# Optimization experiments

Hardware: AMD Instinct MI355X
Metric: run time of the kernel (lower is better)

Reference implementation:

```python
import jax, jax.numpy as jnp
import numpy as np

DIM = 256
NUM_HEADS = 8
NUM_NEI = (16, 32)
G = len(NUM_NEI)          # branches
G_H = NUM_HEADS // G      # heads per branch = 4
G_DIM = DIM // G          # channels per branch = 128
HD = G_DIM // G_H         # head dim = 32
SCALE = HD ** (-0.5)
M_MSF = G                 # MSF branches
CHANNEL = DIM // M_MSF    # 128
D_MSF = CHANNEL           # r=1

gelu = lambda t: jax.nn.gelu(t, approximate=False)


def setup_inputs() -> dict:
    key = jax.random.key(0)
    ks = jax.random.split(key, 16)
    B, N = 4, 2048
    s = lambda fan: fan ** (-0.5)
    inp = {
        "x": jax.random.normal(ks[0], (B, N, DIM), jnp.float32),
        "pos": jax.random.uniform(ks[1], (B, N, 3), jnp.float32),
        # qkv linear (no bias); stored as (in, out)
        "Wqkv": jax.random.normal(ks[2], (DIM, 3 * DIM), jnp.float32) * s(DIM),
        # per-branch rel-pos MLPs: Linear(3, g_dim) + GELU
        "Wp0": jax.random.normal(ks[3], (3, G_DIM), jnp.float32) * s(3),
        "bp0": jnp.zeros((G_DIM,), jnp.float32),
        "Wp1": jax.random.normal(ks[4], (3, G_DIM), jnp.float32) * s(3),
        "bp1": jnp.zeros((G_DIM,), jnp.float32),
        # MSF params
        "W_proj": jax.random.normal(ks[5], (DIM, DIM), jnp.float32) * s(DIM),
        "b_proj": jnp.zeros((DIM,), jnp.float32),
        "W_fc1": jax.random.normal(ks[6], (DIM, D_MSF), jnp.float32) * s(DIM),
        "b_fc1": jnp.zeros((D_MSF,), jnp.float32),
        "W_fc2": jax.random.normal(ks[7], (D_MSF, M_MSF * CHANNEL), jnp.float32) * s(D_MSF),
        "b_fc2": jnp.zeros((M_MSF * CHANNEL,), jnp.float32),
        "W_head": jax.random.normal(ks[8], (DIM, DIM), jnp.float32) * s(DIM),
        "b_head": jnp.zeros((DIM,), jnp.float32),
    }
    return inp


def _branch(q, k, v, pos, knn_idx, Wp, bp):
    """One head-group: KNN gather + rel-pos MLP fused attention.
    q,k,v: [B,N,g_dim]; pos: [B,N,3]; knn_idx: [B,N,nk]."""
    B, N, g_dim = k.shape
    nk = knn_idx.shape[-1]
    gather = jax.vmap(lambda t, idx: t[idx])  # per-batch fancy gather -> [B,N,nk,D]
    knn_xyz = gather(pos, knn_idx)                       # [B,N,nk,3]
    kg = gather(k, knn_idx)                              # [B,N,nk,g_dim]
    vg = gather(v, knn_idx)
    # split heads: b n k (h d) -> b h n k d
    split = lambda t: t.reshape(B, N, nk, G_H, HD).transpose(0, 3, 1, 2, 4)
    kg, vg = split(kg), split(vg)
    rel = pos[:, :, None, :] - knn_xyz                   # [B,N,nk,3]
    vrp = split(gelu(rel @ Wp + bp))                     # [B,h,N,nk,d]
    vg = vg + vrp
    attn_rel = vrp.sum(-1)                               # [B,h,N,nk]
    qh = q.reshape(B, N, G_H, HD).transpose(0, 2, 1, 3)  # [B,h,N,d]
    logits = jnp.einsum('bhnd,bhnkd->bhnk', qh, kg) * SCALE + attn_rel
    a = jax.nn.softmax(logits, axis=-1)
    out = jnp.einsum('bhnk,bhnkd->bhnd', a, vg)          # [B,h,N,d]
    return out.transpose(0, 2, 1, 3).reshape(B, N, g_dim)


def _msf(x, W_proj, b_proj, W_fc1, b_fc1, W_fc2, b_fc2, W_head, b_head):
    bs, N, dim = x.shape
    input_groups = x.transpose(0, 2, 1).reshape(bs, M_MSF, CHANNEL, N)
    feats_proj = gelu(x @ W_proj + b_proj)               # [bs,N,dim]
    feats_S = feats_proj.mean(axis=1)                    # global avg pool over N -> [bs,dim]
    feats_Z = gelu(feats_S @ W_fc1 + b_fc1)
    av = (feats_Z @ W_fc2 + b_fc2).reshape(bs, M_MSF, CHANNEL, 1)
    av = jax.nn.softmax(av, axis=1)                      # softmax over branches
    feats_V = (input_groups * av).reshape(bs, dim, N).transpose(0, 2, 1)
    feats_V = feats_V @ W_head + b_head
    return feats_proj + feats_V


def reference(x, pos, Wqkv, Wp0, bp0, Wp1, bp1,
              W_proj, b_proj, W_fc1, b_fc1, W_fc2, b_fc2, W_head, b_head):
    B, N, C = x.shape
    # pairwise squared distances [B,N,N] (broadcast form, as in source)
    dists = jnp.sum((pos[:, :, None, :] - pos[:, None, :, :]) ** 2, axis=-1)
    order = jnp.argsort(dists, axis=-1)                  # [B,N,N]
    qkv = (x @ Wqkv).reshape(B, N, 3, C).transpose(2, 0, 1, 3)  # [3,B,N,C]
    pos_params = [(Wp0, bp0), (Wp1, bp1)]
    outs = []
    for i, nk in enumerate(NUM_NEI):
        sl = slice(i * G_DIM, (i + 1) * G_DIM)
        q, k, v = qkv[0][..., sl], qkv[1][..., sl], qkv[2][..., sl]
        knn_idx = order[:, :, :nk]
        Wp, bp = pos_params[i]
        outs.append(_branch(q, k, v, pos, knn_idx, Wp, bp))
    xcat = jnp.concatenate(outs, axis=-1)                # [B,N,C]
    return _msf(xcat, W_proj, b_proj, W_fc1, b_fc1, W_fc2, b_fc2, W_head, b_head)
```

## Files before the change

### kernel.cpp

```cpp
#include <hip/hip_runtime.h>
#include <cstdint>
#include <cstddef>

#define B_    4
#define NPT   2048
#define DIM_  256
#define QKVW  768
#define XLEN  2097152
#define QLEN  196608
#define PLEN  65536
#define TOTC  (XLEN + QLEN + 2 * PLEN)

typedef unsigned short ushort_t;
typedef unsigned long long u64;
typedef short bf16x8 __attribute__((ext_vector_type(8)));
typedef float f32x4 __attribute__((ext_vector_type(4)));

__device__ __forceinline__ float gelu_f(float x) {
  return 0.5f * x * (1.0f + erff(x * 0.70710678118654752440f));
}

__device__ __forceinline__ float gelu_fast(float x) {
  const float is2 = 0.70710678118654752440f;
  float z = x * is2;
  float az = __builtin_fabsf(z);
  float t = __builtin_amdgcn_rcpf(fmaf(0.3275911f, az, 1.0f));
  float p = fmaf(1.061405429f, t, -1.453152027f);
  p = fmaf(p, t, 1.421413741f);
  p = fmaf(p, t, -0.284496736f);
  p = fmaf(p, t, 0.254829592f);
  p = p * t;
  float e = __expf(-az * az);
  float er = fmaf(-p, e, 1.0f);
  er = __builtin_copysignf(er, x);
  return 0.5f * x * (1.0f + er);
}

__device__ __forceinline__ ushort_t f2bf(float f) {
  unsigned u = __float_as_uint(f);
  unsigned r = (u + 0x7fffu + ((u >> 16) & 1u)) >> 16;
  return (ushort_t)r;
}
__device__ __forceinline__ float bf2f(ushort_t h) {
  return __uint_as_float(((unsigned)h) << 16);
}

__device__ __forceinline__ float bfly16_sum(float x) {
  x += __int_as_float(__builtin_amdgcn_ds_swizzle(__float_as_int(x), 0x041F));
  x += __int_as_float(__builtin_amdgcn_ds_swizzle(__float_as_int(x), 0x081F));
  x += __int_as_float(__builtin_amdgcn_ds_swizzle(__float_as_int(x), 0x101F));
  x += __int_as_float(__builtin_amdgcn_ds_swizzle(__float_as_int(x), 0x201F));
  return x;
}

__device__ __forceinline__ bf16x8 scale_bf(bf16x8 v, const float* avk) {
  bf16x8 r;
#pragma unroll
  for (int e = 0; e < 8; e++) {
    float f = bf2f((ushort_t)v[e]) * avk[e];
    r[e] = (short)f2bf(f);
  }
  return r;
}

__global__ __launch_bounds__(256) void convert_kernel(
    const float* __restrict__ x, const float* __restrict__ Wqkv,
    const float* __restrict__ Wproj, const float* __restrict__ Whead,
    ushort_t* __restrict__ xbf, ushort_t* __restrict__ WqkvT,
    ushort_t* __restrict__ WprojT, ushort_t* __restrict__ WheadT,
    float* __restrict__ part) {
  int base = blockIdx.x * 256 + threadIdx.x;
  if (base < 1024) part[base] = 0.f;
  for (int i = base; i < TOTC; i += 2048 * 256) {
    if (i < XLEN) {
      xbf[i] = f2bf(x[i]);
    } else if (i < XLEN + QLEN) {
      int e = i - XLEN;
      int k = e / 768, n = e - k * 768;
      WqkvT[n * 256 + k] = f2bf(Wqkv[e]);
    } else if (i < XLEN + QLEN + PLEN) {
      int e = i - XLEN - QLEN;
      int k = e >> 8, n = e & 255;
      WprojT[n * 256 + k] = f2bf(Wproj[e]);
    } else {
      int e = i - XLEN - QLEN - PLEN;
      int k = e >> 8, n = e & 255;
      WheadT[n * 256 + k] = f2bf(Whead[e]);
    }
  }
}

__global__ __launch_bounds__(256) void knn_gemm0_kernel(
    const float* __restrict__ pos, int* __restrict__ idx_out,
    const ushort_t* __restrict__ A, const ushort_t* __restrict__ BT,
    float* __restrict__ C) {
  __shared__ u64 buf[4][128];
  int tid = threadIdx.x;
  int w = tid >> 6, lane = tid & 63;
  if (blockIdx.x >= 2048) {
    constexpr int K = 256;
    constexpr int N = 768;
    int quad = lane >> 4, r16 = lane & 15;
    int t0 = (blockIdx.x - 2048) * 4 + w;
    int m0 = (t0 / 24) * 64, n0 = (t0 % 24) * 32;
    const ushort_t* Ap = A + (size_t)(m0 + r16) * K + quad * 8;
    const ushort_t* Bp = BT + (size_t)(n0 + r16) * K + quad * 8;
    f32x4 acc[4][2] = {};
    bf16x8 af[4], bfv[2], af2[4], bf2[2];
#pragma unroll
    for (int i = 0; i < 4; i++) af[i] = *(const bf16x8*)(Ap + (size_t)i * 16 * K);
#pragma unroll
    for (int j = 0; j < 2; j++) bfv[j] = *(const bf16x8*)(Bp + (size_t)j * 16 * K);
#pragma unroll
    for (int kc = 0; kc < 8; kc++) {
      if (kc < 7) {
        int ko = (kc + 1) * 32;
#pragma unroll
        for (int i = 0; i < 4; i++)
          af2[i] = *(const bf16x8*)(Ap + (size_t)i * 16 * K + ko);
#pragma unroll
        for (int j = 0; j < 2; j++)
          bf2[j] = *(const bf16x8*)(Bp + (size_t)j * 16 * K + ko);
      }
#pragma unroll
      for (int i = 0; i < 4; i++) {
        acc[i][0] = __builtin_amdgcn_mfma_f32_16x16x32_bf16(af[i], bfv[0], acc[i][0], 0, 0, 0);
        acc[i][1] = __builtin_amdgcn_mfma_f32_16x16x32_bf16(af[i], bfv[1], acc[i][1], 0, 0, 0);
      }
#pragma unroll
      for (int i = 0; i < 4; i++) af[i] = af2[i];
      bfv[0] = bf2[0]; bfv[1] = bf2[1];
    }
#pragma unroll
    for (int i = 0; i < 4; i++) {
#pragma unroll
      for (int j = 0; j < 2; j++) {
        int col = n0 + j * 16 + r16;
#pragma unroll
        for (int r = 0; r < 4; r++) {
          int row = m0 + i * 16 + quad * 4 + r;
          C[(size_t)row * N + col] = acc[i][j][r];
        }
      }
    }
    return;
  }
  int wq = blockIdx.x * 4 + w;
  int b = wq >> 11, n = wq & (NPT - 1);
  const float* pb = pos + (size_t)b * NPT * 3;
  float qx = pb[n * 3 + 0], qy = pb[n * 3 + 1], qz = pb[n * 3 + 2];
  float dist[32];
  {
#pragma clang fp contract(off)
#pragma unroll
    for (int s = 0; s < 32; s++) {
      int j = lane + (s << 6);
      float dx = qx - pb[j * 3 + 0];
      float dy = qy - pb[j * 3 + 1];
      float dz = qz - pb[j * 3 + 2];
      float d = dx * dx;
      d = d + dy * dy;
      d = d + dz * dz;
      dist[s] = d;
    }
  }
  unsigned lo = 0x3C000000u;
  unsigned hi = 0x3E800001u;
  for (int it = 0; it < 31 && hi - lo > 1; ++it) {
    unsigned mid = (lo + hi) >> 1;
    float fm = __uint_as_float(mid);
    int c = 0;
#pragma unroll
    for (int s = 0; s < 32; s++)
      c += (int)__popcll(__ballot(dist[s] < fm));
    if (c >= 32) { hi = mid; if (c <= 64) break; }
    else lo = mid;
  }
  float fT = __uint_as_float(hi);
  buf[w][lane] = ~0ULL;
  buf[w][lane + 64] = ~0ULL;
  __builtin_amdgcn_wave_barrier();
  asm volatile("s_waitcnt lgkmcnt(0)" ::: "memory");
  unsigned base = 0;
#pragma unroll
  for (int s = 0; s < 32; s++) {
    bool m = dist[s] < fT;
    u64 bal = __ballot(m);
    unsigned pre = __builtin_amdgcn_mbcnt_hi(
        (unsigned)(bal >> 32), __builtin_amdgcn_mbcnt_lo((unsigned)bal, 0u));
    unsigned p = base + pre;
    if (m && p < 128u) {
      int j = lane + (s << 6);
      buf[w][p] = ((u64)__float_as_uint(dist[s]) << 32) | (unsigned)j;
    }
    base += (unsigned)__popcll(bal);
  }
  __builtin_amdgcn_wave_barrier();
  asm volatile("s_waitcnt lgkmcnt(0)" ::: "memory");
  unsigned total = base;
  if (total > 128u) total = 128u;
  unsigned mt = (total + 7u) & ~7u;
  u64 k0 = buf[w][lane];
  u64 k1 = buf[w][lane + 64];
  int r0 = 0, r1 = 0;
  for (unsigned i = 0; i < mt; i += 8) {
#pragma unroll
    for (int t = 0; t < 8; t++) {
      u64 ki = buf[w][i + t];
      r0 += (ki < k0) ? 1 : 0;
      r1 += (ki < k1) ? 1 : 0;
    }
  }
  if (r0 < 32) idx_out[(size_t)wq * 32 + r0] = (int)(unsigned)(k0 & 0xffffffffULL);
  if (r1 < 32) idx_out[(size_t)wq * 32 + r1] = (int)(unsigned)(k1 & 0xffffffffULL);
}

template <int MODE>
__global__ __launch_bounds__(64, 4) void gemm_rf(
    const ushort_t* __restrict__ A, const ushort_t* __restrict__ BT,
    const float* __restrict__ bias, const float* __restrict__ extra,
    float* __restrict__ C, float* __restrict__ part,
    const float* __restrict__ av, int N) {
  constexpr int K = 256;
  int lane = threadIdx.x;
  int quad = lane >> 4, r16 = lane & 15;
  int t0 = blockIdx.x;
  int m0 = (t0 >> 3) * 64, n0 = (t0 & 7) * 32;
  int batch = m0 >> 11;
  const ushort_t* Ap = A + (size_t)(m0 + r16) * K + quad * 8;
  const ushort_t* Bp = BT + (size_t)(n0 + r16) * K + quad * 8;
  f32x4 acc[4][2] = {};
  bf16x8 af[4], bf[2], af2[4], bf2[2];
#pragma unroll
  for (int i = 0; i < 4; i++) af[i] = *(const bf16x8*)(Ap + (size_t)i * 16 * K);
#pragma unroll
  for (int j = 0; j < 2; j++) bf[j] = *(const bf16x8*)(Bp + (size_t)j * 16 * K);
#pragma unroll
  for (int kc = 0; kc < 8; kc++) {
    if (kc < 7) {
      int ko = (kc + 1) * 32;
#pragma unroll
      for (int i = 0; i < 4; i++)
        af2[i] = *(const bf16x8*)(Ap + (size_t)i * 16 * K + ko);
#pragma unroll
      for (int j = 0; j < 2; j++)
        bf2[j] = *(const bf16x8*)(Bp + (size_t)j * 16 * K + ko);
    }
    bf16x8 b0 = bf[0], b1 = bf[1];
    if (MODE == 2) {
      const float* avk = av + batch * 256 + kc * 32 + quad * 8;
      b0 = scale_bf(b0, avk);
      b1 = scale_bf(b1, avk);
    }
#pragma unroll
    for (int i = 0; i < 4; i++) {
      acc[i][0] = __builtin_amdgcn_mfma_f32_16x16x32_bf16(af[i], b0, acc[i][0], 0, 0, 0);
      acc[i][1] = __builtin_amdgcn_mfma_f32_16x16x32_bf16(af[i], b1, acc[i][1], 0, 0, 0);
    }
#pragma unroll
    for (int i = 0; i < 4; i++) af[i] = af2[i];
    bf[0] = bf2[0]; bf[1] = bf2[1];
  }
  float cs[2] = {};
#pragma unroll
  for (int i = 0; i < 4; i++) {
#pragma unroll
    for (int j = 0; j < 2; j++) {
      int col = n0 + j * 16 + r16;
#pragma unroll
      for (int r = 0; r < 4; r++) {
        int row = m0 + i * 16 + quad * 4 + r;
        float v = acc[i][j][r];
        if (MODE == 1) { v = gelu_fast(v + bias[col]); cs[j] += v; }
        else if (MODE == 2) v = extra[(size_t)row * 256 + col] + v + bias[col];
        C[(size_t)row * N + col] = v;
      }
    }
  }
  if (MODE == 1) {
#pragma unroll
    for (int j = 0; j < 2; j++) {
      cs[j] += __shfl_xor(cs[j], 16, 64);
      cs[j] += __shfl_xor(cs[j], 32, 64);
    }
    if (quad == 0) {
#pragma unroll
      for (int j = 0; j < 2; j++)
        atomicAdd(&part[batch * 256 + n0 + j * 16 + r16], cs[j]);
    }
  }
}

template <int NK>
__device__ __forceinline__ void attn_core(
    const float* __restrict__ kvbase, int c2, const int* sidx,
    const float4* srel, float qSx, float qSy,
    float2 w0, float2 w1, float2 w2, float2 bb,
    float& num0, float& num1, float& den) {
#pragma unroll
  for (int j = 0; j < NK; j++) {
    int jj = __builtin_amdgcn_readfirstlane(sidx[j]);
    float4 rr = srel[j];
    const float* kb = kvbase + (size_t)jj * QKVW;
    float2 kv = *(const float2*)(kb + c2);
    float2 vv = *(const float2*)(kb + 256 + c2);
    float x0 = fmaf(rr.x, w0.x, fmaf(rr.y, w1.x, fmaf(rr.z, w2.x, bb.x)));
    float x1 = fmaf(rr.x, w0.y, fmaf(rr.y, w1.y, fmaf(rr.z, w2.y, bb.y)));
    float z0 = x0 * fmaf(0.0713548163f, x0 * x0, 1.5957691216f);
    float z1 = x1 * fmaf(0.0713548163f, x1 * x1, 1.5957691216f);
    float r0 = x0 * __builtin_amdgcn_rcpf(1.0f + __expf(-z0));
    float r1 = x1 * __builtin_amdgcn_rcpf(1.0f + __expf(-z1));
    float p = fmaf(qSx, kv.x, r0) + fmaf(qSy, kv.y, r1);
    float logit = bfly16_sum(p);
    float e = __expf(logit);
    den += e;
    num0 = fmaf(e, vv.x + r0, num0);
    num1 = fmaf(e, vv.y + r1, num1);
  }
}

__global__ __launch_bounds__(64) void attn_kernel(
    const float* __restrict__ qkv, const float* __restrict__ pos,
    const int* __restrict__ knn,
    const float* __restrict__ Wp0, const float* __restrict__ bp0,
    const float* __restrict__ Wp1, const float* __restrict__ bp1,
    ushort_t* __restrict__ xcat) {
  const float SCALE = 0.17677669529663687f;
  int u = blockIdx.x;
  int g = blockIdx.y;
  int b = u >> 11, n = u & (NPT - 1);
  int lane = threadIdx.x;
  int c2 = lane * 2;
  __shared__ int s_idx[32];
  __shared__ float4 s_rel[32];
  const float* qkvb = qkv + (size_t)b * NPT * QKVW;
  if (lane < 32) {
    int j = knn[(size_t)u * 32 + lane];
    s_idx[lane] = j;
    const float* pn = pos + ((size_t)b * NPT + n) * 3;
    const float* pj = pos + ((size_t)b * NPT + j) * 3;
    s_rel[lane] = make_float4(pn[0] - pj[0], pn[1] - pj[1],
                              pn[2] - pj[2], 0.f);
  }
  __builtin_amdgcn_wave_barrier();
  asm volatile("s_waitcnt lgkmcnt(0)" ::: "memory");
  const float* Wp = g ? Wp1 : Wp0;
  const float* bp = g ? bp1 : bp0;
  float2 w0 = *(const float2*)(Wp + c2);
  float2 w1 = *(const float2*)(Wp + 128 + c2);
  float2 w2 = *(const float2*)(Wp + 256 + c2);
  float2 bb = *(const float2*)(bp + c2);
  float2 q2 = *(const float2*)(qkvb + (size_t)n * QKVW + g * 128 + c2);
  float qSx = q2.x * SCALE, qSy = q2.y * SCALE;
  const float* kvbase = qkvb + 256 + g * 128;
  float num0 = 0.f, num1 = 0.f, den = 0.f;
  if (g == 0)
    attn_core<16>(kvbase, c2, s_idx, s_rel, qSx, qSy, w0, w1, w2, bb,
                  num0, num1, den);
  else
    attn_core<32>(kvbase, c2, s_idx, s_rel, qSx, qSy, w0, w1, w2, bb,
                  num0, num1, den);
  float inv = __builtin_amdgcn_rcpf(den);
  unsigned pk = (unsigned)f2bf(num0 * inv) | ((unsigned)f2bf(num1 * inv) << 16);
  ((unsigned*)xcat)[((size_t)b * NPT + n) * 128 + g * 64 + lane] = pk;
}

__global__ __launch_bounds__(256) void msf_av_kernel(
    const float* __restrict__ part, const float* __restrict__ Wfc1,
    const float* __restrict__ bfc1, const float* __restrict__ Wfc2,
    const float* __restrict__ bfc2, float* __restrict__ av_out) {
  int b = blockIdx.x, t = threadIdx.x;
  __shared__ float S[256], Z[128], A[256];
  S[t] = part[b * 256 + t] * (1.0f / 2048.0f);
  __syncthreads();
  if (t < 128) {
    float z = bfc1[t];
    for (int i = 0; i < 256; i++) z += S[i] * Wfc1[i * 128 + t];
    Z[t] = gelu_f(z);
  }
  __syncthreads();
  float a = bfc2[t];
  for (int j = 0; j < 128; j++) a += Z[j] * Wfc2[j * 256 + t];
  A[t] = a;
  __syncthreads();
  float pA = A[t ^ 128];
  float m = fmaxf(a, pA);
  float e = expf(a - m);
  av_out[b * 256 + t] = e / (e + expf(pA - m));
}

extern "C" void kernel_launch(void* const* d_in, const int* in_sizes, int n_in,
                              void* d_out, int out_size, void* d_ws, size_t ws_size,
                              hipStream_t stream) {
  const float* x     = (const float*)d_in[0];
  const float* pos   = (const float*)d_in[1];
  const float* Wqkv  = (const float*)d_in[2];
  const float* Wp0   = (const float*)d_in[3];
  const float* bp0   = (const float*)d_in[4];
  const float* Wp1   = (const float*)d_in[5];
  const float* bp1   = (const float*)d_in[6];
  const float* Wproj = (const float*)d_in[7];
  const float* bproj = (const float*)d_in[8];
  const float* Wfc1  = (const float*)d_in[9];
  const float* bfc1  = (const float*)d_in[10];
  const float* Wfc2  = (const float*)d_in[11];
  const float* bfc2  = (const float*)d_in[12];
  const float* Whead = (const float*)d_in[13];
  const float* bhead = (const float*)d_in[14];
  float* out = (float*)d_out;

  char* ws = (char*)d_ws;
  size_t off = 0;
  int* idx = (int*)(ws + off);              off += (size_t)B_ * NPT * 32 * 4;
  float* qkv = (float*)(ws + off);          off += (size_t)B_ * NPT * QKVW * 4;
  float* fp = qkv;
  ushort_t* xbf = (ushort_t*)(ws + off);    off += (size_t)B_ * NPT * DIM_ * 2;
  ushort_t* xcat = xbf;
  ushort_t* WqkvT = (ushort_t*)(ws + off);  off += (size_t)QLEN * 2;
  ushort_t* WprojT = (ushort_t*)(ws + off); off += (size_t)PLEN * 2;
  ushort_t* WheadT = (ushort_t*)(ws + off); off += (size_t)PLEN * 2;
  float* part = (float*)(ws + off);         off += 1024 * 4;
  float* av = (float*)(ws + off);           off += 1024 * 4;

  const int M = B_ * NPT;

  convert_kernel<<<2048, 256, 0, stream>>>(x, Wqkv, Wproj, Whead,
                                           xbf, WqkvT, WprojT, WheadT, part);
  knn_gemm0_kernel<<<2048 + 768, 256, 0, stream>>>(pos, idx, xbf, WqkvT, qkv);
  attn_kernel<<<dim3(M, 2), 64, 0, stream>>>(qkv, pos, idx,
                                             Wp0, bp0, Wp1, bp1, xcat);
  gemm_rf<1><<<1024, 64, 0, stream>>>(xcat, WprojT, bproj, nullptr,
                                      fp, part, nullptr, DIM_);
  msf_av_kernel<<<B_, 256, 0, stream>>>(part, Wfc1, bfc1, Wfc2, bfc2, av);
  gemm_rf<2><<<1024, 64, 0, stream>>>(xcat, WheadT, bhead, fp,
                                      out, nullptr, av, DIM_);
}
```

Measured before the change: 191.5 us.

## Store QKV as bf16 and co-schedule GEMM waves with KNN waves per block

New measurement: 185.2 us. 1.03x faster.

```diff
diff --git a/kernel.cpp b/kernel.cpp
--- a/kernel.cpp
+++ b/kernel.cpp
@@ -43,6 +43,12 @@
 }
 __device__ __forceinline__ float bf2f(ushort_t h) {
   return __uint_as_float(((unsigned)h) << 16);
+}
+__device__ __forceinline__ float bflo(unsigned p) {
+  return __uint_as_float(p << 16);
+}
+__device__ __forceinline__ float bfhi(unsigned p) {
+  return __uint_as_float(p & 0xffff0000u);
 }
 
 __device__ __forceinline__ float bfly16_sum(float x) {
@@ -93,15 +99,15 @@
 __global__ __launch_bounds__(256) void knn_gemm0_kernel(
     const float* __restrict__ pos, int* __restrict__ idx_out,
     const ushort_t* __restrict__ A, const ushort_t* __restrict__ BT,
-    float* __restrict__ C) {
-  __shared__ u64 buf[4][128];
+    ushort_t* __restrict__ C) {
+  __shared__ u64 buf[3][128];
   int tid = threadIdx.x;
   int w = tid >> 6, lane = tid & 63;
-  if (blockIdx.x >= 2048) {
+  if (w == 3) {
     constexpr int K = 256;
     constexpr int N = 768;
     int quad = lane >> 4, r16 = lane & 15;
-    int t0 = (blockIdx.x - 2048) * 4 + w;
+    int t0 = blockIdx.x;
     int m0 = (t0 / 24) * 64, n0 = (t0 % 24) * 32;
     const ushort_t* Ap = A + (size_t)(m0 + r16) * K + quad * 8;
     const ushort_t* Bp = BT + (size_t)(n0 + r16) * K + quad * 8;
@@ -139,13 +145,14 @@
 #pragma unroll
         for (int r = 0; r < 4; r++) {
           int row = m0 + i * 16 + quad * 4 + r;
-          C[(size_t)row * N + col] = acc[i][j][r];
+          C[(size_t)row * N + col] = f2bf(acc[i][j][r]);
         }
       }
     }
     return;
   }
-  int wq = blockIdx.x * 4 + w;
+  int wq = blockIdx.x * 3 + w;
+  if (wq >= 8192) return;
   int b = wq >> 11, n = wq & (NPT - 1);
   const float* pb = pos + (size_t)b * NPT * 3;
   float qx = pb[n * 3 + 0], qy = pb[n * 3 + 1], qz = pb[n * 3 + 2];
@@ -293,7 +300,7 @@
 
 template <int NK>
 __device__ __forceinline__ void attn_core(
-    const float* __restrict__ kvbase, int c2, const int* sidx,
+    const ushort_t* __restrict__ kvbase, int lane, const int* sidx,
     const float4* srel, float qSx, float qSy,
     float2 w0, float2 w1, float2 w2, float2 bb,
     float& num0, float& num1, float& den) {
@@ -301,26 +308,28 @@
   for (int j = 0; j < NK; j++) {
     int jj = __builtin_amdgcn_readfirstlane(sidx[j]);
     float4 rr = srel[j];
-    const float* kb = kvbase + (size_t)jj * QKVW;
-    float2 kv = *(const float2*)(kb + c2);
-    float2 vv = *(const float2*)(kb + 256 + c2);
+    const ushort_t* kb = kvbase + (size_t)jj * QKVW;
+    unsigned pk = ((const unsigned*)kb)[lane];
+    unsigned pv = ((const unsigned*)(kb + 256))[lane];
+    float kvx = bflo(pk), kvy = bfhi(pk);
+    float vvx = bflo(pv), vvy = bfhi(pv);
     float x0 = fmaf(rr.x, w0.x, fmaf(rr.y, w1.x, fmaf(rr.z, w2.x, bb.x)));
     float x1 = fmaf(rr.x, w0.y, fmaf(rr.y, w1.y, fmaf(rr.z, w2.y, bb.y)));
     float z0 = x0 * fmaf(0.0713548163f, x0 * x0, 1.5957691216f);
     float z1 = x1 * fmaf(0.0713548163f, x1 * x1, 1.5957691216f);
     float r0 = x0 * __builtin_amdgcn_rcpf(1.0f + __expf(-z0));
     float r1 = x1 * __builtin_amdgcn_rcpf(1.0f + __expf(-z1));
-    float p = fmaf(qSx, kv.x, r0) + fmaf(qSy, kv.y, r1);
+    float p = fmaf(qSx, kvx, r0) + fmaf(qSy, kvy, r1);
     float logit = bfly16_sum(p);
     float e = __expf(logit);
     den += e;
-    num0 = fmaf(e, vv.x + r0, num0);
-    num1 = fmaf(e, vv.y + r1, num1);
+    num0 = fmaf(e, vvx + r0, num0);
+    num1 = fmaf(e, vvy + r1, num1);
   }
 }
 
 __global__ __launch_bounds__(64) void attn_kernel(
-    const float* __restrict__ qkv, const float* __restrict__ pos,
+    const ushort_t* __restrict__ qkv, const float* __restrict__ pos,
     const int* __restrict__ knn,
     const float* __restrict__ Wp0, const float* __restrict__ bp0,
     const float* __restrict__ Wp1, const float* __restrict__ bp1,
@@ -333,7 +342,7 @@
   int c2 = lane * 2;
   __shared__ int s_idx[32];
   __shared__ float4 s_rel[32];
-  const float* qkvb = qkv + (size_t)b * NPT * QKVW;
+  const ushort_t* qkvb = qkv + (size_t)b * NPT * QKVW;
   if (lane < 32) {
     int j = knn[(size_t)u * 32 + lane];
     s_idx[lane] = j;
@@ -350,15 +359,15 @@
   float2 w1 = *(const float2*)(Wp + 128 + c2);
   float2 w2 = *(const float2*)(Wp + 256 + c2);
   float2 bb = *(const float2*)(bp + c2);
-  float2 q2 = *(const float2*)(qkvb + (size_t)n * QKVW + g * 128 + c2);
-  float qSx = q2.x * SCALE, qSy = q2.y * SCALE;
-  const float* kvbase = qkvb + 256 + g * 128;
+  unsigned pq = ((const unsigned*)(qkvb + (size_t)n * QKVW + g * 128))[lane];
+  float qSx = bflo(pq) * SCALE, qSy = bfhi(pq) * SCALE;
+  const ushort_t* kvbase = qkvb + 256 + g * 128;
   float num0 = 0.f, num1 = 0.f, den = 0.f;
   if (g == 0)
-    attn_core<16>(kvbase, c2, s_idx, s_rel, qSx, qSy, w0, w1, w2, bb,
+    attn_core<16>(kvbase, lane, s_idx, s_rel, qSx, qSy, w0, w1, w2, bb,
                   num0, num1, den);
   else
-    attn_core<32>(kvbase, c2, s_idx, s_rel, qSx, qSy, w0, w1, w2, bb,
+    attn_core<32>(kvbase, lane, s_idx, s_rel, qSx, qSy, w0, w1, w2, bb,
                   num0, num1, den);
   float inv = __builtin_amdgcn_rcpf(den);
   unsigned pk = (unsigned)f2bf(num0 * inv) | ((unsigned)f2bf(num1 * inv) << 16);
@@ -412,8 +421,9 @@
   char* ws = (char*)d_ws;
   size_t off = 0;
   int* idx = (int*)(ws + off);              off += (size_t)B_ * NPT * 32 * 4;
-  float* qkv = (float*)(ws + off);          off += (size_t)B_ * NPT * QKVW * 4;
-  float* fp = qkv;
+  ushort_t* qkv = (ushort_t*)(ws + off);
+  float* fp = (float*)(ws + off);
+  off += (size_t)B_ * NPT * QKVW * 4;
   ushort_t* xbf = (ushort_t*)(ws + off);    off += (size_t)B_ * NPT * DIM_ * 2;
   ushort_t* xcat = xbf;
   ushort_t* WqkvT = (ushort_t*)(ws + off);  off += (size_t)QLEN * 2;
@@ -426,7 +436,7 @@
 
   convert_kernel<<<2048, 256, 0, stream>>>(x, Wqkv, Wproj, Whead,
                                            xbf, WqkvT, WprojT, WheadT, part);
-  knn_gemm0_kernel<<<2048 + 768, 256, 0, stream>>>(pos, idx, xbf, WqkvT, qkv);
+  knn_gemm0_kernel<<<3072, 256, 0, stream>>>(pos, idx, xbf, WqkvT, qkv);
   attn_kernel<<<dim3(M, 2), 64, 0, stream>>>(qkv, pos, idx,
                                              Wp0, bp0, Wp1, bp1, xcat);
   gemm_rf<1><<<1024, 64, 0, stream>>>(xcat, WprojT, bproj, nullptr,
```
